# Performance work log

Hardware: AMD Instinct MI355X
Metric: run time of the kernel (lower is better)

## Reference

```python
import jax, jax.numpy as jnp
import numpy as np

B, H, MAX_LEN = 64, 16, 4096
D_KV = 576          # kv_lora_rank (512) + rope dim (64): MLA compressed latent per token
V_DIM = 512         # value read from first kv_lora_rank dims of the latent
SOFTMAX_SCALE = 0.041666666666666664  # 1/sqrt(576)
NEG_INF = -1e30


def setup_inputs() -> dict:
    key = jax.random.key(0)
    k1, k2, k3, k4 = jax.random.split(key, 4)
    query_states = jax.random.normal(k1, (B, H, D_KV), dtype=jnp.float32)
    key_value_states = jax.random.normal(k2, (B, 1, D_KV), dtype=jnp.float32)
    cache = jax.random.normal(k3, (B, MAX_LEN, D_KV), dtype=jnp.float32)
    context_lens = jax.random.randint(k4, (B,), 0, 4095, dtype=jnp.int32)
    return {
        "query_states": query_states,
        "key_value_states": key_value_states,
        "cache": cache,
        "context_lens": context_lens,
    }


def reference(query_states, key_value_states, cache, context_lens):
    # --- update_fusion_cache: scatter the new token's compressed latent into
    # each sequence's slot at position context_lens[b] (decode step, q_len=1).
    b_idx = jnp.arange(B)
    cache = cache.at[b_idx, context_lens].set(key_value_states[:, 0])  # [B, MAX_LEN, D_KV]
    total_lens = context_lens + 1  # valid KV length per sequence after update

    # --- seg_mla_fwd: absorbed MLA attention against the compressed latent cache.
    # scores over full latent (nope+rope) dims; values are first V_DIM dims.
    scores = jnp.einsum("bhd,bsd->bhs", query_states, cache) * SOFTMAX_SCALE  # [B,H,S]
    valid = jnp.arange(MAX_LEN)[None, :] < total_lens[:, None]                # [B,S]
    scores = jnp.where(valid[:, None, :], scores, NEG_INF)
    probs = jax.nn.softmax(scores, axis=-1)                                   # [B,H,S]
    out = jnp.einsum("bhs,bsv->bhv", probs, cache[..., :V_DIM])               # [B,H,V_DIM]
    return out
```

## Files before the change

### kernel.cpp

```cpp
#include <hip/hip_runtime.h>
#include <math.h>


typedef __attribute__((ext_vector_type(8))) short bf16x8;
typedef __attribute__((ext_vector_type(4))) float f32x4;

namespace {
constexpr int NB = 64, NH = 16, MAXLEN = 4096, D = 576, DV = 512;
constexpr int KP = 584;
constexpr int VP = 36;
constexpr int PP = 40;
constexpr float SCALE_LOG2E = 0.041666666666666664f * 1.4426950408889634f;
constexpr float NEGINF = -1e30f;
}

__device__ __forceinline__ uint32_t cvtpk(float a, float b) {
    uint32_t r;
    asm("v_cvt_pk_bf16_f32 %0, %1, %2" : "=v"(r) : "v"(a), "v"(b));
    return r;
}

union FragAB { bf16x8 v; uint32_t u[4]; };

__global__ __launch_bounds__(256, 2)
void mla_mfma(const float* __restrict__ qg, const float* __restrict__ kvnew,
              const float* __restrict__ cache, const int* __restrict__ lens,
              float* __restrict__ ws_o, float* __restrict__ ws_ml,
              int nchunk, int chunk)
{
    const int c = blockIdx.x, b = blockIdx.y;
    const int total = lens[b] + 1;
    const int start = c * chunk;
    if (start >= total) return;
    const int end = min(start + chunk, total);
    const int newpos = total - 1;

    __shared__ short K_s[32 * KP];
    __shared__ short V_s[DV * VP];
    __shared__ short P_s[4 * 16 * PP];

    const int tid  = (int)threadIdx.x;
    const int wave = tid >> 6, lane = tid & 63;
    const int lr = lane & 15, g = lane >> 4;

    const float* vnew = kvnew + (size_t)b * D;
    const float* cb   = cache + (size_t)b * MAXLEN * D;

    const int rg = tid >> 5;
    const int cl = tid & 31;

    float4 nxA[2][4];
    float4 nxB[3][4];

#define ROWPTRS(R0N)                                                           \
        const int gr0 = (R0N) + rg * 4;                                        \
        const int r0c = min(gr0,     MAXLEN - 1);                              \
        const int r1c = min(gr0 + 1, MAXLEN - 1);                              \
        const int r2c = min(gr0 + 2, MAXLEN - 1);                              \
        const int r3c = min(gr0 + 3, MAXLEN - 1);                              \
        const float* s0 = (gr0     == newpos) ? vnew : (cb + (size_t)r0c * D); \
        const float* s1 = (gr0 + 1 == newpos) ? vnew : (cb + (size_t)r1c * D); \
        const float* s2 = (gr0 + 2 == newpos) ? vnew : (cb + (size_t)r2c * D); \
        const float* s3 = (gr0 + 3 == newpos) ? vnew : (cb + (size_t)r3c * D);

#define STAGE_LOAD_A(R0N)                                                      \
    {                                                                          \
        ROWPTRS(R0N)                                                           \
        _Pragma("unroll")                                                      \
        for (int it = 0; it < 2; ++it) {                                       \
            const int cf = 32 * it + cl;                                       \
            nxA[it][0] = *(const float4*)(s0 + cf * 4);                        \
            nxA[it][1] = *(const float4*)(s1 + cf * 4);                        \
            nxA[it][2] = *(const float4*)(s2 + cf * 4);                        \
            nxA[it][3] = *(const float4*)(s3 + cf * 4);                        \
        }                                                                      \
    }

#define STAGE_LOAD_B(R0N)                                                      \
    {                                                                          \
        ROWPTRS(R0N)                                                           \
        _Pragma("unroll")                                                      \
        for (int jt = 0; jt < 3; ++jt) {                                       \
            const int cf = 32 * (jt + 2) + cl;                                 \
            if (cf < 144) {                                                    \
                nxB[jt][0] = *(const float4*)(s0 + cf * 4);                    \
                nxB[jt][1] = *(const float4*)(s1 + cf * 4);                    \
                nxB[jt][2] = *(const float4*)(s2 + cf * 4);                    \
                nxB[jt][3] = *(const float4*)(s3 + cf * 4);                    \
            }                                                                  \
        }                                                                      \
    }

#define WRITE_ONE(NX, CF)                                                      \
    {                                                                          \
        uint2 w;                                                               \
        w.x = cvtpk(NX[0].x, NX[0].y); w.y = cvtpk(NX[0].z, NX[0].w);          \
        *(uint2*)&K_s[(rg * 4 + 0) * KP + (CF) * 4] = w;                       \
        w.x = cvtpk(NX[1].x, NX[1].y); w.y = cvtpk(NX[1].z, NX[1].w);          \
        *(uint2*)&K_s[(rg * 4 + 1) * KP + (CF) * 4] = w;                       \
        w.x = cvtpk(NX[2].x, NX[2].y); w.y = cvtpk(NX[2].z, NX[2].w);          \
        *(uint2*)&K_s[(rg * 4 + 2) * KP + (CF) * 4] = w;                       \
        w.x = cvtpk(NX[3].x, NX[3].y); w.y = cvtpk(NX[3].z, NX[3].w);          \
        *(uint2*)&K_s[(rg * 4 + 3) * KP + (CF) * 4] = w;                       \
        if ((CF) < 128) {                                                      \
            const int v0 = (CF) * 4;                                           \
            w.x = cvtpk(NX[0].x, NX[1].x); w.y = cvtpk(NX[2].x, NX[3].x);      \
            *(uint2*)&V_s[(v0 + 0) * VP + rg * 4] = w;                         \
            w.x = cvtpk(NX[0].y, NX[1].y); w.y = cvtpk(NX[2].y, NX[3].y);      \
            *(uint2*)&V_s[(v0 + 1) * VP + rg * 4] = w;                         \
            w.x = cvtpk(NX[0].z, NX[1].z); w.y = cvtpk(NX[2].z, NX[3].z);      \
            *(uint2*)&V_s[(v0 + 2) * VP + rg * 4] = w;                         \
            w.x = cvtpk(NX[0].w, NX[1].w); w.y = cvtpk(NX[2].w, NX[3].w);      \
            *(uint2*)&V_s[(v0 + 3) * VP + rg * 4] = w;                         \
        }                                                                      \
    }

#define STAGE_WRITE_A()                                                        \
    {                                                                          \
        _Pragma("unroll")                                                      \
        for (int it = 0; it < 2; ++it) {                                       \
            const int cf = 32 * it + cl;                                       \
            WRITE_ONE(nxA[it], cf)                                             \
        }                                                                      \
    }

#define STAGE_WRITE_B()                                                        \
    {                                                                          \
        _Pragma("unroll")                                                      \
        for (int jt = 0; jt < 3; ++jt) {                                       \
            const int cf = 32 * (jt + 2) + cl;                                 \
            if (cf < 144) { WRITE_ONE(nxB[jt], cf) }                           \
        }                                                                      \
    }

    FragAB qf[18];
    {
        const float* qrow = qg + ((size_t)b * NH + lr) * D + g * 8;
        #pragma unroll
        for (int kc = 0; kc < 18; ++kc) {
            float4 x = *(const float4*)(qrow + kc * 32);
            float4 y = *(const float4*)(qrow + kc * 32 + 4);
            qf[kc].u[0] = cvtpk(x.x * SCALE_LOG2E, x.y * SCALE_LOG2E);
            qf[kc].u[1] = cvtpk(x.z * SCALE_LOG2E, x.w * SCALE_LOG2E);
            qf[kc].u[2] = cvtpk(y.x * SCALE_LOG2E, y.y * SCALE_LOG2E);
            qf[kc].u[3] = cvtpk(y.z * SCALE_LOG2E, y.w * SCALE_LOG2E);
        }
    }

    f32x4 acc[8];
    #pragma unroll
    for (int i = 0; i < 8; ++i) acc[i] = (f32x4){0.f, 0.f, 0.f, 0.f};
    float m2[4] = {NEGINF, NEGINF, NEGINF, NEGINF};
    float ll[4] = {0.f, 0.f, 0.f, 0.f};

    STAGE_LOAD_A(start);
    STAGE_LOAD_B(start);
    STAGE_WRITE_A();
    STAGE_WRITE_B();
    __syncthreads();

    for (int r0 = start; r0 < end; r0 += 32) {
        const bool have_next = (r0 + 32 < end);
        if (have_next) STAGE_LOAD_A(r0 + 32);

        f32x4 sc0 = (f32x4){0.f, 0.f, 0.f, 0.f};
        f32x4 sc1 = (f32x4){0.f, 0.f, 0.f, 0.f};
        __builtin_amdgcn_s_setprio(1);
        #pragma unroll
        for (int kc = 0; kc < 18; ++kc) {
            FragAB kb0, kb1;
            kb0.v = *(const bf16x8*)&K_s[lr * KP + kc * 32 + g * 8];
            kb1.v = *(const bf16x8*)&K_s[(16 + lr) * KP + kc * 32 + g * 8];
            sc0 = __builtin_amdgcn_mfma_f32_16x16x32_bf16(qf[kc].v, kb0.v, sc0, 0, 0, 0);
            sc1 = __builtin_amdgcn_mfma_f32_16x16x32_bf16(qf[kc].v, kb1.v, sc1, 0, 0, 0);
        }
        __builtin_amdgcn_s_setprio(0);
        if (r0 + lr >= end)      sc0 = (f32x4){NEGINF, NEGINF, NEGINF, NEGINF};
        if (r0 + 16 + lr >= end) sc1 = (f32x4){NEGINF, NEGINF, NEGINF, NEGINF};

        float mt[4];
        int grew = 0;
        #pragma unroll
        for (int i = 0; i < 4; ++i) {
            float t = fmaxf(sc0[i], sc1[i]);
            t = fmaxf(t, __shfl_xor(t, 1));
            t = fmaxf(t, __shfl_xor(t, 2));
            t = fmaxf(t, __shfl_xor(t, 4));
            t = fmaxf(t, __shfl_xor(t, 8));
            mt[i] = t;
            grew |= (t > m2[i]) ? 1 : 0;
        }
        if (__any(grew)) {
            float scl[4];
            #pragma unroll
            for (int i = 0; i < 4; ++i) {
                const float nm = fmaxf(m2[i], mt[i]);
                scl[i] = exp2f(m2[i] - nm);
                m2[i] = nm;
                ll[i] *= scl[i];
            }
            const f32x4 scl4 = (f32x4){scl[0], scl[1], scl[2], scl[3]};
            #pragma unroll
            for (int vt = 0; vt < 8; ++vt) acc[vt] = acc[vt] * scl4;
        }
        float p0[4], p1[4];
        #pragma unroll
        for (int i = 0; i < 4; ++i) {
            p0[i] = exp2f(sc0[i] - m2[i]);
            p1[i] = exp2f(sc1[i] - m2[i]);
            ll[i] += p0[i] + p1[i];
        }

        short* pw = &P_s[wave * 16 * PP];
        #pragma unroll
        for (int i = 0; i < 4; ++i) {
            pw[(4 * g + i) * PP + lr]      = (short)cvtpk(p0[i], p0[i]);
            pw[(4 * g + i) * PP + 16 + lr] = (short)cvtpk(p1[i], p1[i]);
        }
        asm volatile("s_waitcnt lgkmcnt(0)" ::: "memory");
        FragAB pa;
        pa.v = *(const bf16x8*)&pw[lr * PP + g * 8];

        __builtin_amdgcn_s_setprio(1);
        #pragma unroll
        for (int vt = 0; vt < 8; ++vt) {
            const int v = wave * 128 + vt * 16 + lr;
            FragAB vb;
            *(uint2*)&vb.u[0] = *(const uint2*)&V_s[v * VP + g * 8];
            *(uint2*)&vb.u[2] = *(const uint2*)&V_s[v * VP + g * 8 + 4];
            acc[vt] = __builtin_amdgcn_mfma_f32_16x16x32_bf16(pa.v, vb.v, acc[vt], 0, 0, 0);
        }
        __builtin_amdgcn_s_setprio(0);

        if (have_next) STAGE_LOAD_B(r0 + 32);
        __syncthreads();
        if (have_next) { STAGE_WRITE_A(); STAGE_WRITE_B(); }
        __syncthreads();
    }

    #pragma unroll
    for (int i = 0; i < 4; ++i) {
        float s = ll[i];
        s += __shfl_xor(s, 1);
        s += __shfl_xor(s, 2);
        s += __shfl_xor(s, 4);
        s += __shfl_xor(s, 8);
        ll[i] = s;
    }

    float* ob = ws_o + (((size_t)b * nchunk + c) * NH) * DV;
    #pragma unroll
    for (int vt = 0; vt < 8; ++vt) {
        const int v = wave * 128 + vt * 16 + lr;
        #pragma unroll
        for (int i = 0; i < 4; ++i)
            ob[(4 * g + i) * DV + v] = acc[vt][i];
    }
    if (wave == 0 && lr == 0) {
        float* mlb = ws_ml + ((size_t)b * nchunk + c) * NH * 2;
        #pragma unroll
        for (int i = 0; i < 4; ++i) {
            mlb[(4 * g + i) * 2]     = m2[i];
            mlb[(4 * g + i) * 2 + 1] = ll[i];
        }
    }
#undef STAGE_LOAD_A
#undef STAGE_LOAD_B
#undef STAGE_WRITE_A
#undef STAGE_WRITE_B
#undef WRITE_ONE
#undef ROWPTRS
}

__global__ __launch_bounds__(256)
void mla_reduce(const int* __restrict__ lens,
                const float* __restrict__ ws_o,
                const float* __restrict__ ws_ml,
                float* __restrict__ out,
                int nchunk, int chunk)
{
    const int h = blockIdx.x;
    const int b = blockIdx.y;
    const int tid = (int)threadIdx.x;
    const int total = lens[b] + 1;
    const int nact = min(nchunk, (total + chunk - 1) / chunk);

    float M = NEGINF;
    {
        int c = 0;
        for (; c + 4 <= nact; c += 4) {
            const float m0 = ws_ml[(((size_t)b * nchunk + c    ) * NH + h) * 2];
            const float m1 = ws_ml[(((size_t)b * nchunk + c + 1) * NH + h) * 2];
            const float m2_ = ws_ml[(((size_t)b * nchunk + c + 2) * NH + h) * 2];
            const float m3 = ws_ml[(((size_t)b * nchunk + c + 3) * NH + h) * 2];
            M = fmaxf(M, fmaxf(fmaxf(m0, m1), fmaxf(m2_, m3)));
        }
        for (; c < nact; ++c)
            M = fmaxf(M, ws_ml[(((size_t)b * nchunk + c) * NH + h) * 2]);
    }

    float a0 = 0.f, a1 = 0.f, L = 0.f;
    {
        int c = 0;
        for (; c + 2 <= nact; c += 2) {
            const size_t mlb0 = (((size_t)b * nchunk + c    ) * NH + h) * 2;
            const size_t mlb1 = (((size_t)b * nchunk + c + 1) * NH + h) * 2;
            const float w0 = exp2f(ws_ml[mlb0] - M);
            const float w1 = exp2f(ws_ml[mlb1] - M);
            const float2 o0 = *(const float2*)&ws_o[
                (((size_t)b * nchunk + c    ) * NH + h) * (size_t)DV + 2 * tid];
            const float2 o1 = *(const float2*)&ws_o[
                (((size_t)b * nchunk + c + 1) * NH + h) * (size_t)DV + 2 * tid];
            L += w0 * ws_ml[mlb0 + 1] + w1 * ws_ml[mlb1 + 1];
            a0 = fmaf(w1, o1.x, fmaf(w0, o0.x, a0));
            a1 = fmaf(w1, o1.y, fmaf(w0, o0.y, a1));
        }
        for (; c < nact; ++c) {
            const size_t mlb = (((size_t)b * nchunk + c) * NH + h) * 2;
            const float w = exp2f(ws_ml[mlb] - M);
            L += w * ws_ml[mlb + 1];
            const float2 o = *(const float2*)&ws_o[
                (((size_t)b * nchunk + c) * NH + h) * (size_t)DV + 2 * tid];
            a0 = fmaf(w, o.x, a0);
            a1 = fmaf(w, o.y, a1);
        }
    }
    const float inv = 1.f / L;
    *(float2*)&out[((size_t)b * NH + h) * (size_t)DV + 2 * tid] =
        make_float2(a0 * inv, a1 * inv);
}

extern "C" void kernel_launch(void* const* d_in, const int* in_sizes, int n_in,
                              void* d_out, int out_size, void* d_ws, size_t ws_size,
                              hipStream_t stream)
{
    (void)in_sizes; (void)n_in; (void)out_size;
    const float* qg    = (const float*)d_in[0];
    const float* kvnew = (const float*)d_in[1];
    const float* cache = (const float*)d_in[2];
    const int*   lens  = (const int*)d_in[3];
    float* out = (float*)d_out;

    int nchunk = 32;
    while (nchunk > 1 &&
           (size_t)NB * nchunk * NH * (DV + 2) * sizeof(float) > ws_size)
        nchunk >>= 1;
    const int chunk = MAXLEN / nchunk;

    float* ws_o  = (float*)d_ws;
    float* ws_ml = ws_o + (size_t)NB * nchunk * NH * DV;

    dim3 gA(nchunk, NB);
    mla_mfma<<<gA, 256, 0, stream>>>(qg, kvnew, cache, lens, ws_o, ws_ml,
                                     nchunk, chunk);
    dim3 gB(NH, NB);
    mla_reduce<<<gB, 256, 0, stream>>>(lens, ws_o, ws_ml, out, nchunk, chunk);
}
```

Baseline: 138.5 us.

## Drop transposed V tile, read V from swizzled K tile, raise occupancy

Removes the separate transposed V shared-memory buffer and instead gathers the value fragments from the K tile with per-element 16-bit LDS reads. An XOR swizzle is applied to the K tile columns to reduce bank conflicts. The register prefetch double-buffering is dropped in favour of a simple load-sync-compute loop, and launch bounds go from 2 to 3 blocks per CU. Less LDS and fewer registers per block should allow more concurrent blocks to hide memory latency. The cost is losing the explicit load/compute overlap and issuing many more narrow LDS reads for V.

Result: slower. 296.2 us (+113.9%).

```diff
diff --git a/kernel.cpp b/kernel.cpp
--- a/kernel.cpp
+++ b/kernel.cpp
@@ -8,7 +8,6 @@
 namespace {
 constexpr int NB = 64, NH = 16, MAXLEN = 4096, D = 576, DV = 512;
 constexpr int KP = 584;
-constexpr int VP = 36;
 constexpr int PP = 40;
 constexpr float SCALE_LOG2E = 0.041666666666666664f * 1.4426950408889634f;
 constexpr float NEGINF = -1e30f;
@@ -22,7 +21,7 @@
 
 union FragAB { bf16x8 v; uint32_t u[4]; };
 
-__global__ __launch_bounds__(256, 2)
+__global__ __launch_bounds__(256, 3)
 void mla_mfma(const float* __restrict__ qg, const float* __restrict__ kvnew,
               const float* __restrict__ cache, const int* __restrict__ lens,
               float* __restrict__ ws_o, float* __restrict__ ws_ml,
@@ -36,7 +35,6 @@
     const int newpos = total - 1;
 
     __shared__ short K_s[32 * KP];
-    __shared__ short V_s[DV * VP];
     __shared__ short P_s[4 * 16 * PP];
 
     const int tid  = (int)threadIdx.x;
@@ -48,90 +46,6 @@
 
     const int rg = tid >> 5;
     const int cl = tid & 31;
-
-    float4 nxA[2][4];
-    float4 nxB[3][4];
-
-#define ROWPTRS(R0N)                                                           \
-        const int gr0 = (R0N) + rg * 4;                                        \
-        const int r0c = min(gr0,     MAXLEN - 1);                              \
-        const int r1c = min(gr0 + 1, MAXLEN - 1);                              \
-        const int r2c = min(gr0 + 2, MAXLEN - 1);                              \
-        const int r3c = min(gr0 + 3, MAXLEN - 1);                              \
-        const float* s0 = (gr0     == newpos) ? vnew : (cb + (size_t)r0c * D); \
-        const float* s1 = (gr0 + 1 == newpos) ? vnew : (cb + (size_t)r1c * D); \
-        const float* s2 = (gr0 + 2 == newpos) ? vnew : (cb + (size_t)r2c * D); \
-        const float* s3 = (gr0 + 3 == newpos) ? vnew : (cb + (size_t)r3c * D);
-
-#define STAGE_LOAD_A(R0N)                                                      \
-    {                                                                          \
-        ROWPTRS(R0N)                                                           \
-        _Pragma("unroll")                                                      \
-        for (int it = 0; it < 2; ++it) {                                       \
-            const int cf = 32 * it + cl;                                       \
-            nxA[it][0] = *(const float4*)(s0 + cf * 4);                        \
-            nxA[it][1] = *(const float4*)(s1 + cf * 4);                        \
-            nxA[it][2] = *(const float4*)(s2 + cf * 4);                        \
-            nxA[it][3] = *(const float4*)(s3 + cf * 4);                        \
-        }                                                                      \
-    }
-
-#define STAGE_LOAD_B(R0N)                                                      \
-    {                                                                          \
-        ROWPTRS(R0N)                                                           \
-        _Pragma("unroll")                                                      \
-        for (int jt = 0; jt < 3; ++jt) {                                       \
-            const int cf = 32 * (jt + 2) + cl;                                 \
-            if (cf < 144) {                                                    \
-                nxB[jt][0] = *(const float4*)(s0 + cf * 4);                    \
-                nxB[jt][1] = *(const float4*)(s1 + cf * 4);                    \
-                nxB[jt][2] = *(const float4*)(s2 + cf * 4);                    \
-                nxB[jt][3] = *(const float4*)(s3 + cf * 4);                    \
-            }                                                                  \
-        }                                                                      \
-    }
-
-#define WRITE_ONE(NX, CF)                                                      \
-    {                                                                          \
-        uint2 w;                                                               \
-        w.x = cvtpk(NX[0].x, NX[0].y); w.y = cvtpk(NX[0].z, NX[0].w);          \
-        *(uint2*)&K_s[(rg * 4 + 0) * KP + (CF) * 4] = w;                       \
-        w.x = cvtpk(NX[1].x, NX[1].y); w.y = cvtpk(NX[1].z, NX[1].w);          \
-        *(uint2*)&K_s[(rg * 4 + 1) * KP + (CF) * 4] = w;                       \
-        w.x = cvtpk(NX[2].x, NX[2].y); w.y = cvtpk(NX[2].z, NX[2].w);          \
-        *(uint2*)&K_s[(rg * 4 + 2) * KP + (CF) * 4] = w;                       \
-        w.x = cvtpk(NX[3].x, NX[3].y); w.y = cvtpk(NX[3].z, NX[3].w);          \
-        *(uint2*)&K_s[(rg * 4 + 3) * KP + (CF) * 4] = w;                       \
-        if ((CF) < 128) {                                                      \
-            const int v0 = (CF) * 4;                                           \
-            w.x = cvtpk(NX[0].x, NX[1].x); w.y = cvtpk(NX[2].x, NX[3].x);      \
-            *(uint2*)&V_s[(v0 + 0) * VP + rg * 4] = w;                         \
-            w.x = cvtpk(NX[0].y, NX[1].y); w.y = cvtpk(NX[2].y, NX[3].y);      \
-            *(uint2*)&V_s[(v0 + 1) * VP + rg * 4] = w;                         \
-            w.x = cvtpk(NX[0].z, NX[1].z); w.y = cvtpk(NX[2].z, NX[3].z);      \
-            *(uint2*)&V_s[(v0 + 2) * VP + rg * 4] = w;                         \
-            w.x = cvtpk(NX[0].w, NX[1].w); w.y = cvtpk(NX[2].w, NX[3].w);      \
-            *(uint2*)&V_s[(v0 + 3) * VP + rg * 4] = w;                         \
-        }                                                                      \
-    }
-
-#define STAGE_WRITE_A()                                                        \
-    {                                                                          \
-        _Pragma("unroll")                                                      \
-        for (int it = 0; it < 2; ++it) {                                       \
-            const int cf = 32 * it + cl;                                       \
-            WRITE_ONE(nxA[it], cf)                                             \
-        }                                                                      \
-    }
-
-#define STAGE_WRITE_B()                                                        \
-    {                                                                          \
-        _Pragma("unroll")                                                      \
-        for (int jt = 0; jt < 3; ++jt) {                                       \
-            const int cf = 32 * (jt + 2) + cl;                                 \
-            if (cf < 144) { WRITE_ONE(nxB[jt], cf) }                           \
-        }                                                                      \
-    }
 
     FragAB qf[18];
     {
@@ -153,24 +67,55 @@
     float m2[4] = {NEGINF, NEGINF, NEGINF, NEGINF};
     float ll[4] = {0.f, 0.f, 0.f, 0.f};
 
-    STAGE_LOAD_A(start);
-    STAGE_LOAD_B(start);
-    STAGE_WRITE_A();
-    STAGE_WRITE_B();
-    __syncthreads();
+    const int swz_st = (rg >> 1) << 4;
+    const int sw0 = (lr >> 3) << 4;
+    const int sw1 = ((16 + lr) >> 3) << 4;
 
     for (int r0 = start; r0 < end; r0 += 32) {
-        const bool have_next = (r0 + 32 < end);
-        if (have_next) STAGE_LOAD_A(r0 + 32);
+        __syncthreads();
+
+        {
+            const int gr0 = r0 + rg * 4;
+            const int r0c = min(gr0,     MAXLEN - 1);
+            const int r1c = min(gr0 + 1, MAXLEN - 1);
+            const int r2c = min(gr0 + 2, MAXLEN - 1);
+            const int r3c = min(gr0 + 3, MAXLEN - 1);
+            const float* s0 = (gr0     == newpos) ? vnew : (cb + (size_t)r0c * D);
+            const float* s1 = (gr0 + 1 == newpos) ? vnew : (cb + (size_t)r1c * D);
+            const float* s2 = (gr0 + 2 == newpos) ? vnew : (cb + (size_t)r2c * D);
+            const float* s3 = (gr0 + 3 == newpos) ? vnew : (cb + (size_t)r3c * D);
+            #pragma unroll
+            for (int it = 0; it < 5; ++it) {
+                const int cf = 32 * it + cl;
+                if (cf < 144) {
+                    const int cs = (cf * 4) ^ swz_st;
+                    float4 x0 = *(const float4*)(s0 + cf * 4);
+                    float4 x1 = *(const float4*)(s1 + cf * 4);
+                    float4 x2 = *(const float4*)(s2 + cf * 4);
+                    float4 x3 = *(const float4*)(s3 + cf * 4);
+                    uint2 w;
+                    w.x = cvtpk(x0.x, x0.y); w.y = cvtpk(x0.z, x0.w);
+                    *(uint2*)&K_s[(rg * 4 + 0) * KP + cs] = w;
+                    w.x = cvtpk(x1.x, x1.y); w.y = cvtpk(x1.z, x1.w);
+                    *(uint2*)&K_s[(rg * 4 + 1) * KP + cs] = w;
+                    w.x = cvtpk(x2.x, x2.y); w.y = cvtpk(x2.z, x2.w);
+                    *(uint2*)&K_s[(rg * 4 + 2) * KP + cs] = w;
+                    w.x = cvtpk(x3.x, x3.y); w.y = cvtpk(x3.z, x3.w);
+                    *(uint2*)&K_s[(rg * 4 + 3) * KP + cs] = w;
+                }
+            }
+        }
+        __syncthreads();
 
         f32x4 sc0 = (f32x4){0.f, 0.f, 0.f, 0.f};
         f32x4 sc1 = (f32x4){0.f, 0.f, 0.f, 0.f};
         __builtin_amdgcn_s_setprio(1);
         #pragma unroll
         for (int kc = 0; kc < 18; ++kc) {
+            const int col = kc * 32 + g * 8;
             FragAB kb0, kb1;
-            kb0.v = *(const bf16x8*)&K_s[lr * KP + kc * 32 + g * 8];
-            kb1.v = *(const bf16x8*)&K_s[(16 + lr) * KP + kc * 32 + g * 8];
+            kb0.v = *(const bf16x8*)&K_s[lr * KP + (col ^ sw0)];
+            kb1.v = *(const bf16x8*)&K_s[(16 + lr) * KP + (col ^ sw1)];
             sc0 = __builtin_amdgcn_mfma_f32_16x16x32_bf16(qf[kc].v, kb0.v, sc0, 0, 0, 0);
             sc1 = __builtin_amdgcn_mfma_f32_16x16x32_bf16(qf[kc].v, kb1.v, sc1, 0, 0, 0);
         }
@@ -224,18 +169,18 @@
         __builtin_amdgcn_s_setprio(1);
         #pragma unroll
         for (int vt = 0; vt < 8; ++vt) {
-            const int v = wave * 128 + vt * 16 + lr;
+            const int vcol = (wave * 128 + vt * 16 + lr) ^ (g << 4);
             FragAB vb;
-            *(uint2*)&vb.u[0] = *(const uint2*)&V_s[v * VP + g * 8];
-            *(uint2*)&vb.u[2] = *(const uint2*)&V_s[v * VP + g * 8 + 4];
+            #pragma unroll
+            for (int j2 = 0; j2 < 4; ++j2) {
+                union { short s[2]; uint32_t u; } t;
+                t.s[0] = K_s[(g * 8 + 2 * j2)     * KP + vcol];
+                t.s[1] = K_s[(g * 8 + 2 * j2 + 1) * KP + vcol];
+                vb.u[j2] = t.u;
+            }
             acc[vt] = __builtin_amdgcn_mfma_f32_16x16x32_bf16(pa.v, vb.v, acc[vt], 0, 0, 0);
         }
         __builtin_amdgcn_s_setprio(0);
-
-        if (have_next) STAGE_LOAD_B(r0 + 32);
-        __syncthreads();
-        if (have_next) { STAGE_WRITE_A(); STAGE_WRITE_B(); }
-        __syncthreads();
     }
 
     #pragma unroll
@@ -264,12 +209,6 @@
             mlb[(4 * g + i) * 2 + 1] = ll[i];
         }
     }
-#undef STAGE_LOAD_A
-#undef STAGE_LOAD_B
-#undef STAGE_WRITE_A
-#undef STAGE_WRITE_B
-#undef WRITE_ONE
-#undef ROWPTRS
 }
 
 __global__ __launch_bounds__(256)
```
